# Optimization experiments

Measured on AMD Instinct MI355X. Metric: run time of the kernel, lower is better.

The kernel has to match this reference:

```python
import jax, jax.numpy as jnp
import numpy as np

B, T, L, H, NH, F, V, K = 8, 128, 12, 768, 12, 3072, 30522, 5
DH = H // NH
START, STOP = 3, 4  # tag_to_idx['<START>'], tag_to_idx['<STOP>']


def _ln(x, s, b):
    m = jnp.mean(x, -1, keepdims=True)
    v = jnp.var(x, -1, keepdims=True)
    return (x - m) * jax.lax.rsqrt(v + 1e-12) * s + b


def setup_inputs() -> dict:
    key = jax.random.key(0)
    ks = jax.random.split(key, 16)
    sc = 0.02
    rn = lambda k, shp: jax.random.normal(k, shp, jnp.float32) * sc
    inp = {
        'sentence': jax.random.randint(ks[0], (B, T), 0, V),
        'sentence_mask': jnp.ones((B, T), jnp.int32),
        'word_emb': rn(ks[1], (V, H)),
        'pos_emb': rn(ks[2], (T, H)),
        'type_emb': rn(ks[3], (2, H)),
        'emb_ln_s': jnp.ones((H,), jnp.float32),
        'emb_ln_b': jnp.zeros((H,), jnp.float32),
        'Wqkv': rn(ks[4], (L, H, 3 * H)), 'bqkv': jnp.zeros((L, 3 * H), jnp.float32),
        'Wo': rn(ks[5], (L, H, H)), 'bo': jnp.zeros((L, H), jnp.float32),
        'ln1_s': jnp.ones((L, H), jnp.float32), 'ln1_b': jnp.zeros((L, H), jnp.float32),
        'W1': rn(ks[6], (L, H, F)), 'b1': jnp.zeros((L, F), jnp.float32),
        'W2': rn(ks[7], (L, F, H)), 'b2': jnp.zeros((L, H), jnp.float32),
        'ln2_s': jnp.ones((L, H), jnp.float32), 'ln2_b': jnp.zeros((L, H), jnp.float32),
        'Wt': rn(ks[8], (H, K)), 'bt': jnp.zeros((K,), jnp.float32),
    }
    trans = jax.random.normal(ks[9], (K, K), jnp.float32)
    # transitions[START, :] = -10000 ; transitions[:, STOP] = -10000
    trans = trans.at[START, :].set(-10000.0).at[:, STOP].set(-10000.0)
    inp['transitions'] = trans
    return inp


def _bert_feats(sentence, sentence_mask, word_emb, pos_emb, type_emb,
                emb_ln_s, emb_ln_b, Wqkv, bqkv, Wo, bo, ln1_s, ln1_b,
                W1, b1, W2, b2, ln2_s, ln2_b, Wt, bt):
    # embeddings (token_type_ids=None -> all zeros)
    x = word_emb[sentence] + pos_emb[None, :, :] + type_emb[0][None, None, :]
    x = _ln(x, emb_ln_s, emb_ln_b)
    # additive attention bias from padding mask
    bias = (1.0 - sentence_mask.astype(jnp.float32))[:, None, None, :] * -10000.0
    inv_sqrt_dh = 1.0 / np.sqrt(DH)

    def layer(h, p):
        wqkv, bqk, wo, bo_, s1, sb1, w1, wb1, w2, wb2, s2, sb2 = p
        qkv = h @ wqkv + bqk
        q, k, v = jnp.split(qkv, 3, axis=-1)
        q = q.reshape(B, T, NH, DH)
        k = k.reshape(B, T, NH, DH)
        v = v.reshape(B, T, NH, DH)
        att = jnp.einsum('bqhd,bkhd->bhqk', q, k) * inv_sqrt_dh + bias
        att = jax.nn.softmax(att, axis=-1)
        ctx = jnp.einsum('bhqk,bkhd->bqhd', att, v).reshape(B, T, H)
        h = _ln(h + ctx @ wo + bo_, s1, sb1)
        ff = jax.nn.gelu(h @ w1 + wb1) @ w2 + wb2
        h = _ln(h + ff, s2, sb2)
        return h, None

    x, _ = jax.lax.scan(layer, x, (Wqkv, bqkv, Wo, bo, ln1_s, ln1_b,
                                   W1, b1, W2, b2, ln2_s, ln2_b))
    # dropout(p=0.2) is identity at inference
    return x @ Wt + bt  # [B, T, K]


def _viterbi(feats, transitions):
    # feats: [B, T, K]; transitions[to, from]
    init = jnp.full((B, K), -10000.0, feats.dtype).at[:, START].set(0.0)

    def fwd_step(ld, feat_t):
        m = transitions[None, :, :] + ld[:, None, :]  # [B, K(to), K(from)]
        best = jnp.max(m, axis=-1)
        psi_t = jnp.argmax(m, axis=-1)
        return best + feat_t, psi_t

    feats_t = jnp.swapaxes(feats, 0, 1)  # [T, B, K]
    ld, psis = jax.lax.scan(fwd_step, init, feats_t[1:])  # psis: [T-1, B, K]
    score = jnp.max(ld, axis=-1)          # [B]
    last = jnp.argmax(ld, axis=-1)        # [B]

    def bwd_step(p, psi_t):
        prev = jnp.take_along_axis(psi_t, p[:, None], axis=-1)[:, 0]
        return prev, prev

    _, rest = jax.lax.scan(bwd_step, last, psis, reverse=True)  # [T-1, B]
    path = jnp.concatenate([rest, last[None, :]], axis=0).T     # [B, T]
    return score, path


def reference(sentence, sentence_mask, word_emb, pos_emb, type_emb,
              emb_ln_s, emb_ln_b, Wqkv, bqkv, Wo, bo, ln1_s, ln1_b,
              W1, b1, W2, b2, ln2_s, ln2_b, Wt, bt, transitions):
    feats = _bert_feats(sentence, sentence_mask, word_emb, pos_emb, type_emb,
                        emb_ln_s, emb_ln_b, Wqkv, bqkv, Wo, bo, ln1_s, ln1_b,
                        W1, b1, W2, b2, ln2_s, ln2_b, Wt, bt)
    score, path = _viterbi(feats, transitions)
    return score, path
```

## Files before the change

kernel.cpp:

```cpp
#include <hip/hip_runtime.h>
#include <cstdint>
#include <cstddef>

#define BB 8
#define TT 128
#define LL 12
#define HH 768
#define NHH 12
#define DHH 64
#define FFI 3072
#define KT 5
#define START_TAG 3
#define MTOK (BB*TT)

typedef _Float16 f16x8 __attribute__((ext_vector_type(8)));
typedef _Float16 f16x4 __attribute__((ext_vector_type(4)));
typedef float f32x4 __attribute__((ext_vector_type(4)));

__device__ __forceinline__ void gl_lds16(const _Float16* g, _Float16* l) {
    __builtin_amdgcn_global_load_lds(
        (const __attribute__((address_space(1))) unsigned int*)g,
        (__attribute__((address_space(3))) unsigned int*)l, 16, 0, 0);
}

__device__ __forceinline__ float gelu_f(float x) {
    float c = 0.7978845608028654f * (x + 0.044715f * x * x * x);
    return 0.5f * x * (1.f + tanhf(c));
}

__device__ __forceinline__ void write_h_planes(const float* rowbuf, int tok,
                                               _Float16* dh, _Float16* dl, int c) {
    int kb = c >> 2;
    int rowm = tok & 127, mb = tok >> 7;
    int koct = c & 3;
    int p = rowm * 4 + (koct ^ (rowm & 3));
    size_t tb = ((size_t)(mb * 24 + kb)) * 4096;
    f16x8 vh, vl;
#pragma unroll
    for (int j = 0; j < 8; ++j) {
        float x = rowbuf[c * 8 + j];
        _Float16 hi = (_Float16)x;
        vh[j] = hi;
        vl[j] = (_Float16)((x - (float)hi) * 4096.f);
    }
    *(f16x8*)(dh + tb + (size_t)p * 8) = vh;
    *(f16x8*)(dl + tb + (size_t)p * 8) = vl;
}

__global__ __launch_bounds__(256) void embed_ln_kernel(
    const int* __restrict__ sentence,
    const float* __restrict__ word_emb,
    const float* __restrict__ pos_emb,
    const float* __restrict__ type_emb,
    const float* __restrict__ ln_s,
    const float* __restrict__ ln_b,
    float* __restrict__ h,
    _Float16* __restrict__ dh, _Float16* __restrict__ dl)
{
    int tok = blockIdx.x;
    int t = tok % TT;
    int id = sentence[tok];
    const float* we = word_emb + (size_t)id * HH;
    const float* pe = pos_emb + (size_t)t * HH;

    __shared__ float rowbuf[HH];
    __shared__ float rs_[4], rss_[4];
    float x[3];
    float s = 0.f, ss = 0.f;
#pragma unroll
    for (int i = 0; i < 3; ++i) {
        int d = threadIdx.x + i * 256;
        float v = we[d] + pe[d] + type_emb[d];
        x[i] = v; s += v; ss += v * v;
    }
    for (int o = 32; o; o >>= 1) { s += __shfl_down(s, o); ss += __shfl_down(ss, o); }
    int wid = threadIdx.x >> 6;
    if ((threadIdx.x & 63) == 0) { rs_[wid] = s; rss_[wid] = ss; }
    __syncthreads();
    s = rs_[0] + rs_[1] + rs_[2] + rs_[3];
    ss = rss_[0] + rss_[1] + rss_[2] + rss_[3];
    float mean = s * (1.f / HH);
    float var = ss * (1.f / HH) - mean * mean;
    float rstd = rsqrtf(var + 1e-12f);
#pragma unroll
    for (int i = 0; i < 3; ++i) {
        int d = threadIdx.x + i * 256;
        float y = (x[i] - mean) * rstd * ln_s[d] + ln_b[d];
        h[(size_t)tok * HH + d] = y;
        rowbuf[d] = y;
    }
    __syncthreads();
    if (threadIdx.x < 96) write_h_planes(rowbuf, tok, dh, dl, threadIdx.x);
}

__global__ __launch_bounds__(256) void add_ln_red_kernel(
    float* __restrict__ h, const float* __restrict__ parts,
    const float* __restrict__ bias,
    const float* __restrict__ ln_s, const float* __restrict__ ln_b,
    _Float16* __restrict__ dh, _Float16* __restrict__ dl)
{
    int tok = blockIdx.x;
    __shared__ float rowbuf[HH];
    __shared__ float rs_[4], rss_[4];
    float x[3];
    float s = 0.f, ss = 0.f;
#pragma unroll
    for (int i = 0; i < 3; ++i) {
        int d = threadIdx.x + i * 256;
        size_t idx = (size_t)tok * HH + d;
        float delta = parts[idx] + parts[idx + (size_t)MTOK * HH]
                    + parts[idx + 2 * (size_t)MTOK * HH] + parts[idx + 3 * (size_t)MTOK * HH]
                    + bias[d];
        float v = h[idx] + delta;
        x[i] = v; s += v; ss += v * v;
    }
    for (int o = 32; o; o >>= 1) { s += __shfl_down(s, o); ss += __shfl_down(ss, o); }
    int wid = threadIdx.x >> 6;
    if ((threadIdx.x & 63) == 0) { rs_[wid] = s; rss_[wid] = ss; }
    __syncthreads();
    s = rs_[0] + rs_[1] + rs_[2] + rs_[3];
    ss = rss_[0] + rss_[1] + rss_[2] + rss_[3];
    float mean = s * (1.f / HH);
    float var = ss * (1.f / HH) - mean * mean;
    float rstd = rsqrtf(var + 1e-12f);
#pragma unroll
    for (int i = 0; i < 3; ++i) {
        int d = threadIdx.x + i * 256;
        float y = (x[i] - mean) * rstd * ln_s[d] + ln_b[d];
        h[(size_t)tok * HH + d] = y;
        rowbuf[d] = y;
    }
    __syncthreads();
    if (threadIdx.x < 96) write_h_planes(rowbuf, tok, dh, dl, threadIdx.x);
}

__global__ __launch_bounds__(256) void wconv_kernel(
    const float* __restrict__ Wqkv, const float* __restrict__ Wo,
    const float* __restrict__ W1, const float* __restrict__ W2,
    _Float16* __restrict__ qh, _Float16* __restrict__ ql,
    _Float16* __restrict__ oh, _Float16* __restrict__ ol,
    _Float16* __restrict__ f1h, _Float16* __restrict__ f1l,
    _Float16* __restrict__ f2h, _Float16* __restrict__ f2l)
{
    int b = blockIdx.x;
    const float* src; _Float16 *dh, *dl; int N, kTi, idx;
    if (b < 864)       { idx = b;        src = Wqkv; dh = qh;  dl = ql;  N = 2304; kTi = 24; }
    else if (b < 1152) { idx = b - 864;  src = Wo;   dh = oh;  dl = ol;  N = 768;  kTi = 24; }
    else if (b < 2304) { idx = b - 1152; src = W1;   dh = f1h; dl = f1l; N = 3072; kTi = 24; }
    else               { idx = b - 2304; src = W2;   dh = f2h; dl = f2l; N = 768;  kTi = 96; }
    int nb = idx / kTi, kb = idx % kTi;

    __shared__ float tile[32][65];
    const float* s0 = src + (size_t)(kb * 32) * N + nb * 64;
#pragma unroll
    for (int i = 0; i < 8; ++i) {
        int q = threadIdx.x + i * 256;
        int kk = q >> 6, n = q & 63;
        tile[kk][n] = s0[(size_t)kk * N + n];
    }
    __syncthreads();
    int p = threadIdx.x;
    int n = p >> 2, koct = (p & 3) ^ (n & 3);
    f16x8 vh, vl;
#pragma unroll
    for (int j = 0; j < 8; ++j) {
        float x = tile[koct * 8 + j][n];
        _Float16 hi = (_Float16)x;
        vh[j] = hi;
        vl[j] = (_Float16)((x - (float)hi) * 4096.f);
    }
    size_t tb = (size_t)idx * 2048;
    *(f16x8*)(dh + tb + (size_t)p * 8) = vh;
    *(f16x8*)(dl + tb + (size_t)p * 8) = vl;
}

template<int MODE>
__global__ __launch_bounds__(256) void mfma_gemm(
    const _Float16* __restrict__ Ah, const _Float16* __restrict__ Al,
    const _Float16* __restrict__ Bh, const _Float16* __restrict__ Bl,
    const float* __restrict__ bias, float* __restrict__ outF,
    _Float16* __restrict__ o1h, _Float16* __restrict__ o1l,
    _Float16* __restrict__ o2h, _Float16* __restrict__ o2l,
    int N, int kTi, int kpz)
{
    constexpr bool TRANS = (MODE >= 2);
    __shared__ _Float16 lds[2][12288];
    int tid = threadIdx.x, lane = tid & 63, w = tid >> 6;
    int wm = w >> 1, wn = w & 1;
    int mb = blockIdx.y, nb = blockIdx.x;
    int ktBeg = TRANS ? 0 : blockIdx.z * kpz;
    int ktEnd = TRANS ? kTi : ktBeg + kpz;

    const _Float16 *aTh, *aTl, *bTh, *bTl;
    if constexpr (!TRANS) {
        aTh = Ah + (size_t)mb * kTi * 4096;
        aTl = Al + (size_t)mb * kTi * 4096;
        bTh = Bh + (size_t)nb * kTi * 2048;
        bTl = Bl + (size_t)nb * kTi * 2048;
    } else {
        aTh = Ah + (size_t)(2 * mb) * kTi * 2048;
        aTl = Al + (size_t)(2 * mb) * kTi * 2048;
        bTh = Bh + (size_t)(nb >> 1) * kTi * 4096 + (nb & 1) * 2048;
        bTl = Bl + (size_t)(nb >> 1) * kTi * 4096 + (nb & 1) * 2048;
    }

    f32x4 acch[4][2], accc[4][2];
#pragma unroll
    for (int i = 0; i < 4; ++i)
#pragma unroll
        for (int j = 0; j < 2; ++j) { acch[i][j] = (f32x4)0.f; accc[i][j] = (f32x4)0.f; }

    auto stage = [&](int buf, int kt) {
#pragma unroll
        for (int j = 0; j < 6; ++j) {
            int i = w * 6 + j;
            const _Float16* src;
            if constexpr (!TRANS) {
                if (i < 8)       src = aTh + (size_t)kt * 4096 + i * 512;
                else if (i < 16) src = aTl + (size_t)kt * 4096 + (i - 8) * 512;
                else if (i < 20) src = bTh + (size_t)kt * 2048 + (i - 16) * 512;
                else             src = bTl + (size_t)kt * 2048 + (i - 20) * 512;
            } else {
                if (i < 8)       src = aTh + (size_t)(i >> 2) * kTi * 2048 + (size_t)kt * 2048 + (i & 3) * 512;
                else if (i < 16) src = aTl + (size_t)((i - 8) >> 2) * kTi * 2048 + (size_t)kt * 2048 + ((i - 8) & 3) * 512;
                else if (i < 20) src = bTh + (size_t)kt * 4096 + (i - 16) * 512;
                else             src = bTl + (size_t)kt * 4096 + (i - 20) * 512;
            }
            gl_lds16(src + lane * 8, &lds[buf][i * 512]);
        }
    };

    stage(0, ktBeg);
    __syncthreads();
    int buf = 0;
    int lm = lane & 15, lk = lane >> 4;
    for (int kt = ktBeg; kt < ktEnd; ++kt) {
        if (kt + 1 < ktEnd) stage(buf ^ 1, kt + 1);
        const char* lb = (const char*)&lds[buf][0];
        f16x8 ahf[4], alf[4], bhf[2], blf[2];
#pragma unroll
        for (int mi = 0; mi < 4; ++mi) {
            int row = wm * 64 + mi * 16 + lm;
            int off = (row * 64 + lk * 16) ^ ((row & 3) << 4);
            ahf[mi] = *(const f16x8*)(lb + off);
            alf[mi] = *(const f16x8*)(lb + 8192 + off);
        }
#pragma unroll
        for (int ni = 0; ni < 2; ++ni) {
            int nr = wn * 32 + ni * 16 + lm;
            int off = (nr * 64 + lk * 16) ^ ((nr & 3) << 4);
            bhf[ni] = *(const f16x8*)(lb + 16384 + off);
            blf[ni] = *(const f16x8*)(lb + 20480 + off);
        }
#pragma unroll
        for (int mi = 0; mi < 4; ++mi)
#pragma unroll
            for (int ni = 0; ni < 2; ++ni) {
                acch[mi][ni] = __builtin_amdgcn_mfma_f32_16x16x32_f16(ahf[mi], bhf[ni], acch[mi][ni], 0, 0, 0);
                accc[mi][ni] = __builtin_amdgcn_mfma_f32_16x16x32_f16(ahf[mi], blf[ni], accc[mi][ni], 0, 0, 0);
                accc[mi][ni] = __builtin_amdgcn_mfma_f32_16x16x32_f16(alf[mi], bhf[ni], accc[mi][ni], 0, 0, 0);
            }
        __syncthreads();
        buf ^= 1;
    }

    const float inv = 1.0f / 4096.0f;
    if constexpr (MODE == 0) {
        float* Cz = outF + (size_t)blockIdx.z * 1024 * N;
#pragma unroll
        for (int mi = 0; mi < 4; ++mi)
#pragma unroll
            for (int ni = 0; ni < 2; ++ni) {
                int col = nb * 64 + wn * 32 + ni * 16 + lm;
                int r0 = mb * 128 + wm * 64 + mi * 16 + lk * 4;
#pragma unroll
                for (int j = 0; j < 4; ++j)
                    Cz[(size_t)(r0 + j) * N + col] = acch[mi][ni][j] + accc[mi][ni][j] * inv;
            }
    } else if constexpr (MODE == 2) {
        int region = mb / 6;
#pragma unroll
        for (int mi = 0; mi < 4; ++mi)
#pragma unroll
            for (int ni = 0; ni < 2; ++ni) {
                int n = mb * 128 + wm * 64 + mi * 16 + lk * 4;
                int tok = nb * 64 + wn * 32 + ni * 16 + lm;
                float4 bv = *(const float4*)(bias + n);
                float v[4];
#pragma unroll
                for (int j = 0; j < 4; ++j)
                    v[j] = acch[mi][ni][j] + accc[mi][ni][j] * inv + (&bv.x)[j];
                int b = tok >> 7, q = tok & 127;
                if (region < 2) {
                    int hh2 = (n >> 6) % 12, d = n & 63;
                    size_t img = (size_t)(b * 12 + hh2);
                    _Float16* dsth = (region == 0) ? o1h : o2h;
                    _Float16* dstl = (region == 0) ? o1l : o2l;
                    int byteo = q * 128 + ((d * 2) ^ ((q & 7) << 4));
                    f16x4 hi, lo;
#pragma unroll
                    for (int j = 0; j < 4; ++j) {
                        _Float16 hv = (_Float16)v[j];
                        hi[j] = hv; lo[j] = (_Float16)((v[j] - (float)hv) * 4096.f);
                    }
                    *(f16x4*)((char*)dsth + img * 16384 + byteo) = hi;
                    *(f16x4*)((char*)dstl + img * 16384 + byteo) = lo;
                } else {
                    int hh2 = (n - 1536) >> 6, d = n & 63;
                    float* vdst = outF + (size_t)(b * 12 + hh2) * 8192;
#pragma unroll
                    for (int j = 0; j < 4; ++j)
                        vdst[(size_t)(d + j) * 128 + q] = v[j];
                }
            }
    } else {
#pragma unroll
        for (int mi = 0; mi < 4; ++mi)
#pragma unroll
            for (int ni = 0; ni < 2; ++ni) {
                int n = mb * 128 + wm * 64 + mi * 16 + lk * 4;
                int tok = nb * 64 + wn * 32 + ni * 16 + lm;
                float4 bv = *(const float4*)(bias + n);
                int mbt = tok >> 7, rowm = tok & 127;
                int kb = n >> 5, koct = (n >> 3) & 3, half = (n >> 2) & 1;
                size_t eo = ((size_t)(mbt * 96 + kb)) * 4096
                          + (size_t)(rowm * 4 + (koct ^ (rowm & 3))) * 8 + half * 4;
                f16x4 hi, lo;
#pragma unroll
                for (int j = 0; j < 4; ++j) {
                    float x = gelu_f(acch[mi][ni][j] + accc[mi][ni][j] * inv + (&bv.x)[j]);
                    _Float16 hv = (_Float16)x;
                    hi[j] = hv; lo[j] = (_Float16)((x - (float)hv) * 4096.f);
                }
                *(f16x4*)(o1h + eo) = hi;
                *(f16x4*)(o1l + eo) = lo;
            }
    }
}

__global__ __launch_bounds__(256, 1) void attn_mfma(
    const _Float16* __restrict__ Qp_h, const _Float16* __restrict__ Qp_l,
    const _Float16* __restrict__ Kp_h, const _Float16* __restrict__ Kp_l,
    const float* __restrict__ vT, const int* __restrict__ mask,
    _Float16* __restrict__ cA_h, _Float16* __restrict__ cA_l)
{
    __shared__ __align__(16) char sm[98816];
    char* Kh = sm;            char* Klo = sm + 16384;
    char* Qh = sm + 32768;    char* Qlo = sm + 49152;
    char* Ph = sm;            char* Plo = sm + 32768;
    char* Vth = sm + 65536;   char* Vtl = sm + 81920;
    float* biasf = (float*)(sm + 98304);

    int bx = blockIdx.x; int b = bx / 12, h = bx % 12;
    int tid = threadIdx.x, lane = tid & 63, wv = tid >> 6;
    int lm = lane & 15, g = lane >> 4;
    const float inv = 1.0f / 4096.0f;

    {
        const _Float16* srcs[4] = { Kp_h + (size_t)bx * 8192, Kp_l + (size_t)bx * 8192,
                                    Qp_h + (size_t)bx * 8192, Qp_l + (size_t)bx * 8192 };
        char* dsts[4] = { Kh, Klo, Qh, Qlo };
#pragma unroll
        for (int p = 0; p < 4; ++p)
#pragma unroll
            for (int r = 0; r < 4; ++r) {
                int cbase = r * 256 + wv * 64;
                gl_lds16(srcs[p] + (size_t)(cbase + lane) * 8, (_Float16*)(dsts[p] + (size_t)cbase * 16));
            }
    }
    if (tid < 128) biasf[tid] = (1.f - (float)mask[b * 128 + tid]) * -10000.f;
    __syncthreads();

    f32x4 ah[8][2], ac[8][2];
#pragma unroll
    for (int i = 0; i < 8; ++i)
#pragma unroll
        for (int j = 0; j < 2; ++j) { ah[i][j] = (f32x4)0.f; ac[i][j] = (f32x4)0.f; }
#pragma unroll
    for (int ks = 0; ks < 2; ++ks) {
        f16x8 qf[2][2];
#pragma unroll
        for (int nf = 0; nf < 2; ++nf) {
            int q = wv * 32 + nf * 16 + lm;
            int off = (q * 128 + ks * 64 + g * 16) ^ ((q & 7) << 4);
            qf[nf][0] = *(const f16x8*)(Qh + off);
            qf[nf][1] = *(const f16x8*)(Qlo + off);
        }
#pragma unroll
        for (int mf = 0; mf < 8; ++mf) {
            int kt = mf * 16 + lm;
            int off = (kt * 128 + ks * 64 + g * 16) ^ ((kt & 7) << 4);
            f16x8 kh = *(const f16x8*)(Kh + off);
            f16x8 kl = *(const f16x8*)(Klo + off);
#pragma unroll
            for (int nf = 0; nf < 2; ++nf) {
                ah[mf][nf] = __builtin_amdgcn_mfma_f32_16x16x32_f16(kh, qf[nf][0], ah[mf][nf], 0, 0, 0);
                ac[mf][nf] = __builtin_amdgcn_mfma_f32_16x16x32_f16(kh, qf[nf][1], ac[mf][nf], 0, 0, 0);
                ac[mf][nf] = __builtin_amdgcn_mfma_f32_16x16x32_f16(kl, qf[nf][0], ac[mf][nf], 0, 0, 0);
            }
        }
    }

    float kb_[8][4];
#pragma unroll
    for (int mf = 0; mf < 8; ++mf)
#pragma unroll
        for (int jj = 0; jj < 4; ++jj) kb_[mf][jj] = biasf[mf * 16 + g * 4 + jj];

    float pv_[2][8][4], rs_[2];
#pragma unroll
    for (int nf = 0; nf < 2; ++nf) {
        float mx = -1e30f;
#pragma unroll
        for (int mf = 0; mf < 8; ++mf)
#pragma unroll
            for (int jj = 0; jj < 4; ++jj) {
                float s = (ah[mf][nf][jj] + ac[mf][nf][jj] * inv) * 0.125f + kb_[mf][jj];
                pv_[nf][mf][jj] = s;
                mx = fmaxf(mx, s);
            }
        mx = fmaxf(mx, __shfl_xor(mx, 16));
        mx = fmaxf(mx, __shfl_xor(mx, 32));
        float sum = 0.f;
#pragma unroll
        for (int mf = 0; mf < 8; ++mf)
#pragma unroll
            for (int jj = 0; jj < 4; ++jj) {
                float e = expf(pv_[nf][mf][jj] - mx);
                pv_[nf][mf][jj] = e;
                sum += e;
            }
        sum += __shfl_xor(sum, 16);
        sum += __shfl_xor(sum, 32);
        rs_[nf] = 1.f / sum;
    }
    __syncthreads();

#pragma unroll
    for (int nf = 0; nf < 2; ++nf) {
        int q = wv * 32 + nf * 16 + lm;
#pragma unroll
        for (int mf = 0; mf < 8; ++mf) {
            f16x4 hi, lo;
#pragma unroll
            for (int jj = 0; jj < 4; ++jj) {
                float p = pv_[nf][mf][jj] * rs_[nf];
                _Float16 hv = (_Float16)p;
                hi[jj] = hv; lo[jj] = (_Float16)((p - (float)hv) * 4096.f);
            }
            int byteo = (q * 256 + mf * 32 + g * 8) ^ ((q & 7) << 4);
            *(f16x4*)(Ph + byteo) = hi;
            *(f16x4*)(Plo + byteo) = lo;
        }
    }
    {
        int d = tid >> 2, tb = (tid & 3) * 32;
        const float* vsrc = vT + (size_t)bx * 8192 + (size_t)d * 128 + tb;
#pragma unroll
        for (int i = 0; i < 8; ++i) {
            float4 v = *(const float4*)(vsrc + i * 4);
            f16x4 hi, lo;
#pragma unroll
            for (int jj = 0; jj < 4; ++jj) {
                float x = (&v.x)[jj];
                _Float16 hv = (_Float16)x;
                hi[jj] = hv; lo[jj] = (_Float16)((x - (float)hv) * 4096.f);
            }
            int byteo = (d * 256 + (tb + i * 4) * 2) ^ ((d & 7) << 4);
            *(f16x4*)(Vth + byteo) = hi;
            *(f16x4*)(Vtl + byteo) = lo;
        }
    }
    __syncthreads();

    f32x4 ch[4][2], cc[4][2];
#pragma unroll
    for (int i = 0; i < 4; ++i)
#pragma unroll
        for (int j = 0; j < 2; ++j) { ch[i][j] = (f32x4)0.f; cc[i][j] = (f32x4)0.f; }
#pragma unroll
    for (int ks = 0; ks < 4; ++ks) {
        f16x8 pf[2][2];
#pragma unroll
        for (int nf = 0; nf < 2; ++nf) {
            int q = wv * 32 + nf * 16 + lm;
            int off = (q * 256 + ks * 64 + g * 16) ^ ((q & 7) << 4);
            pf[nf][0] = *(const f16x8*)(Ph + off);
            pf[nf][1] = *(const f16x8*)(Plo + off);
        }
#pragma unroll
        for (int mf = 0; mf < 4; ++mf) {
            int d = mf * 16 + lm;
            int off = (d * 256 + ks * 64 + g * 16) ^ ((d & 7) << 4);
            f16x8 vh = *(const f16x8*)(Vth + off);
            f16x8 vl = *(const f16x8*)(Vtl + off);
#pragma unroll
            for (int nf = 0; nf < 2; ++nf) {
                ch[mf][nf] = __builtin_amdgcn_mfma_f32_16x16x32_f16(vh, pf[nf][0], ch[mf][nf], 0, 0, 0);
                cc[mf][nf] = __builtin_amdgcn_mfma_f32_16x16x32_f16(vh, pf[nf][1], cc[mf][nf], 0, 0, 0);
                cc[mf][nf] = __builtin_amdgcn_mfma_f32_16x16x32_f16(vl, pf[nf][0], cc[mf][nf], 0, 0, 0);
            }
        }
    }

#pragma unroll
    for (int mf = 0; mf < 4; ++mf)
#pragma unroll
        for (int nf = 0; nf < 2; ++nf) {
            int q = wv * 32 + nf * 16 + lm;
            int d0 = mf * 16 + g * 4;
            f16x4 hi, lo;
#pragma unroll
            for (int jj = 0; jj < 4; ++jj) {
                float x = ch[mf][nf][jj] + cc[mf][nf][jj] * inv;
                _Float16 hv = (_Float16)x;
                hi[jj] = hv; lo[jj] = (_Float16)((x - (float)hv) * 4096.f);
            }
            int kb = h * 2 + (d0 >> 5), koct = (d0 >> 3) & 3, half = (d0 >> 2) & 1;
            size_t eo = ((size_t)(b * 24 + kb)) * 4096
                      + (size_t)(q * 4 + (koct ^ (q & 3))) * 8 + half * 4;
            *(f16x4*)(cA_h + eo) = hi;
            *(f16x4*)(cA_l + eo) = lo;
        }
}

__global__ __launch_bounds__(320) void feats_kernel(
    const float* __restrict__ h, const float* __restrict__ Wt,
    const float* __restrict__ bt, float* __restrict__ feats)
{
    int tok = blockIdx.x;
    int w = threadIdx.x / 64, lane = threadIdx.x % 64;
    float s = 0.f;
    for (int d = lane; d < HH; d += 64)
        s += h[(size_t)tok * HH + d] * Wt[d * KT + w];
    for (int o = 32; o; o >>= 1) s += __shfl_down(s, o);
    if (lane == 0) feats[tok * KT + w] = s + bt[w];
}

__global__ __launch_bounds__(64) void viterbi_kernel(
    const float* __restrict__ feats, const float* __restrict__ trans,
    float* __restrict__ out)
{
    __shared__ float tr[KT][KT];
    __shared__ unsigned char psi[TT - 1][BB][KT];
    int tid = threadIdx.x;
    if (tid < KT * KT) tr[tid / KT][tid % KT] = trans[tid];
    __syncthreads();
    if (tid < BB) {
        int b = tid;
        float ld[KT];
#pragma unroll
        for (int k = 0; k < KT; ++k) ld[k] = (k == START_TAG) ? 0.f : -10000.f;
        for (int t = 1; t < TT; ++t) {
            float nld[KT];
#pragma unroll
            for (int to = 0; to < KT; ++to) {
                float best = tr[to][0] + ld[0];
                int arg = 0;
#pragma unroll
                for (int fr = 1; fr < KT; ++fr) {
                    float v = tr[to][fr] + ld[fr];
                    if (v > best) { best = v; arg = fr; }
                }
                psi[t - 1][b][to] = (unsigned char)arg;
                nld[to] = best + feats[(size_t)(b * TT + t) * KT + to];
            }
#pragma unroll
            for (int k = 0; k < KT; ++k) ld[k] = nld[k];
        }
        float sc = ld[0]; int last = 0;
#pragma unroll
        for (int k = 1; k < KT; ++k) if (ld[k] > sc) { sc = ld[k]; last = k; }
        out[b] = sc;
        int p = last;
        out[BB + b * TT + (TT - 1)] = (float)last;
        for (int t = TT - 2; t >= 0; --t) {
            p = psi[t][b][p];
            out[BB + b * TT + t] = (float)p;
        }
    }
}

extern "C" void kernel_launch(void* const* d_in, const int* in_sizes, int n_in,
                              void* d_out, int out_size, void* d_ws, size_t ws_size,
                              hipStream_t stream) {
    const int*   sentence = (const int*)d_in[0];
    const int*   mask     = (const int*)d_in[1];
    const float* word_emb = (const float*)d_in[2];
    const float* pos_emb  = (const float*)d_in[3];
    const float* type_emb = (const float*)d_in[4];
    const float* emb_ln_s = (const float*)d_in[5];
    const float* emb_ln_b = (const float*)d_in[6];
    const float* Wqkv     = (const float*)d_in[7];
    const float* bqkv     = (const float*)d_in[8];
    const float* Wo       = (const float*)d_in[9];
    const float* bo       = (const float*)d_in[10];
    const float* ln1_s    = (const float*)d_in[11];
    const float* ln1_b    = (const float*)d_in[12];
    const float* W1       = (const float*)d_in[13];
    const float* b1       = (const float*)d_in[14];
    const float* W2       = (const float*)d_in[15];
    const float* b2       = (const float*)d_in[16];
    const float* ln2_s    = (const float*)d_in[17];
    const float* ln2_b    = (const float*)d_in[18];
    const float* Wt       = (const float*)d_in[19];
    const float* bt       = (const float*)d_in[20];
    const float* trans    = (const float*)d_in[21];

    char* base = (char*)d_ws;
    size_t off = 0;
    auto alloc = [&](size_t bytes) { void* p = base + off; off += (bytes + 255) & ~(size_t)255; return p; };

    _Float16* wq_h = (_Float16*)alloc(768u * 2304 * 2);
    _Float16* wq_l = (_Float16*)alloc(768u * 2304 * 2);
    _Float16* wo_h = (_Float16*)alloc(768u * 768 * 2);
    _Float16* wo_l = (_Float16*)alloc(768u * 768 * 2);
    _Float16* w1_h = (_Float16*)alloc(768u * 3072 * 2);
    _Float16* w1_l = (_Float16*)alloc(768u * 3072 * 2);
    _Float16* w2_h = (_Float16*)alloc(3072u * 768 * 2);
    _Float16* w2_l = (_Float16*)alloc(3072u * 768 * 2);
    float* h       = (float*)alloc((size_t)MTOK * HH * 4);
    _Float16* hA_h = (_Float16*)alloc((size_t)MTOK * HH * 2);
    _Float16* hA_l = (_Float16*)alloc((size_t)MTOK * HH * 2);
    _Float16* Qp_h = (_Float16*)alloc((size_t)96 * 8192 * 2);
    _Float16* Qp_l = (_Float16*)alloc((size_t)96 * 8192 * 2);
    _Float16* Kp_h = (_Float16*)alloc((size_t)96 * 8192 * 2);
    _Float16* Kp_l = (_Float16*)alloc((size_t)96 * 8192 * 2);
    float* vT      = (float*)alloc((size_t)96 * 8192 * 4);
    _Float16* cA_h = (_Float16*)alloc((size_t)MTOK * HH * 2);
    _Float16* cA_l = (_Float16*)alloc((size_t)MTOK * HH * 2);
    _Float16* gA_h = (_Float16*)alloc((size_t)MTOK * FFI * 2);
    _Float16* gA_l = (_Float16*)alloc((size_t)MTOK * FFI * 2);
    float* parts   = (float*)alloc((size_t)4 * MTOK * HH * 4);
    float* featsb  = (float*)alloc((size_t)MTOK * KT * 4);

    embed_ln_kernel<<<MTOK, 256, 0, stream>>>(sentence, word_emb, pos_emb, type_emb,
                                              emb_ln_s, emb_ln_b, h, hA_h, hA_l);
    for (int l = 0; l < LL; ++l) {
        wconv_kernel<<<3456, 256, 0, stream>>>(
            Wqkv + (size_t)l * 768 * 2304, Wo + (size_t)l * 768 * 768,
            W1 + (size_t)l * 768 * 3072, W2 + (size_t)l * 3072 * 768,
            wq_h, wq_l, wo_h, wo_l, w1_h, w1_l, w2_h, w2_l);
        mfma_gemm<2><<<dim3(16, 18), 256, 0, stream>>>(
            wq_h, wq_l, hA_h, hA_l, bqkv + (size_t)l * 2304, vT,
            Qp_h, Qp_l, Kp_h, Kp_l, 0, 24, 24);
        attn_mfma<<<96, 256, 0, stream>>>(Qp_h, Qp_l, Kp_h, Kp_l, vT, mask, cA_h, cA_l);
        mfma_gemm<0><<<dim3(12, 8, 4), 256, 0, stream>>>(
            cA_h, cA_l, wo_h, wo_l, nullptr, parts,
            nullptr, nullptr, nullptr, nullptr, 768, 24, 6);
        add_ln_red_kernel<<<MTOK, 256, 0, stream>>>(
            h, parts, bo + (size_t)l * HH, ln1_s + (size_t)l * HH, ln1_b + (size_t)l * HH, hA_h, hA_l);
        mfma_gemm<3><<<dim3(16, 24), 256, 0, stream>>>(
            w1_h, w1_l, hA_h, hA_l, b1 + (size_t)l * FFI, nullptr,
            gA_h, gA_l, nullptr, nullptr, 0, 24, 24);
        mfma_gemm<0><<<dim3(12, 8, 4), 256, 0, stream>>>(
            gA_h, gA_l, w2_h, w2_l, nullptr, parts,
            nullptr, nullptr, nullptr, nullptr, 768, 96, 24);
        add_ln_red_kernel<<<MTOK, 256, 0, stream>>>(
            h, parts, b2 + (size_t)l * HH, ln2_s + (size_t)l * HH, ln2_b + (size_t)l * HH, hA_h, hA_l);
    }
    feats_kernel<<<MTOK, 320, 0, stream>>>(h, Wt, bt, featsb);
    viterbi_kernel<<<1, 64, 0, stream>>>(featsb, trans, (float*)d_out);
}
```

Baseline: 1.496 ms.

## Batch weight conversion for all layers and fuse final LN with tag projection

When the workspace is large enough, all twelve layers' fp32 weights are split into fp16 hi/lo planes by a single up-front conversion launch instead of one launch per layer. This removes eleven launches and lets the conversion run as one large grid. The last layer's add+LayerNorm kernel is also templated to compute the 5-tag emission features directly, which drops the separate feats kernel and the final h write. The cost is a much larger workspace footprint, and the GEMM row-stride arguments change from 0 to explicit values, which may alter how the weight operand is addressed.

```diff
diff --git a/kernel.cpp b/kernel.cpp
--- a/kernel.cpp
+++ b/kernel.cpp
@@ -12,6 +12,11 @@
 #define KT 5
 #define START_TAG 3
 #define MTOK (BB*TT)
+
+#define LQS 1769472u
+#define LOS 589824u
+#define L1S 2359296u
+#define L2S 2359296u
 
 typedef _Float16 f16x8 __attribute__((ext_vector_type(8)));
 typedef _Float16 f16x4 __attribute__((ext_vector_type(4)));
@@ -93,11 +98,14 @@
     if (threadIdx.x < 96) write_h_planes(rowbuf, tok, dh, dl, threadIdx.x);
 }
 
+template<int FEATS>
 __global__ __launch_bounds__(256) void add_ln_red_kernel(
     float* __restrict__ h, const float* __restrict__ parts,
     const float* __restrict__ bias,
     const float* __restrict__ ln_s, const float* __restrict__ ln_b,
-    _Float16* __restrict__ dh, _Float16* __restrict__ dl)
+    _Float16* __restrict__ dh, _Float16* __restrict__ dl,
+    const float* __restrict__ Wt, const float* __restrict__ bt,
+    float* __restrict__ feats)
 {
     int tok = blockIdx.x;
     __shared__ float rowbuf[HH];
@@ -123,17 +131,45 @@
     float mean = s * (1.f / HH);
     float var = ss * (1.f / HH) - mean * mean;
     float rstd = rsqrtf(var + 1e-12f);
+    float yv[3];
 #pragma unroll
     for (int i = 0; i < 3; ++i) {
         int d = threadIdx.x + i * 256;
         float y = (x[i] - mean) * rstd * ln_s[d] + ln_b[d];
-        h[(size_t)tok * HH + d] = y;
-        rowbuf[d] = y;
-    }
-    __syncthreads();
-    if (threadIdx.x < 96) write_h_planes(rowbuf, tok, dh, dl, threadIdx.x);
-}
-
+        yv[i] = y;
+        if constexpr (!FEATS) {
+            h[(size_t)tok * HH + d] = y;
+            rowbuf[d] = y;
+        }
+    }
+    if constexpr (!FEATS) {
+        __syncthreads();
+        if (threadIdx.x < 96) write_h_planes(rowbuf, tok, dh, dl, threadIdx.x);
+    } else {
+        float pt[5] = {0.f, 0.f, 0.f, 0.f, 0.f};
+#pragma unroll
+        for (int i = 0; i < 3; ++i) {
+            int d = threadIdx.x + i * 256;
+#pragma unroll
+            for (int t = 0; t < 5; ++t) pt[t] += yv[i] * Wt[d * 5 + t];
+        }
+#pragma unroll
+        for (int t = 0; t < 5; ++t)
+            for (int o = 32; o; o >>= 1) pt[t] += __shfl_down(pt[t], o);
+        __shared__ float fred[4][5];
+        if ((threadIdx.x & 63) == 0)
+#pragma unroll
+            for (int t = 0; t < 5; ++t) fred[wid][t] = pt[t];
+        __syncthreads();
+        if (threadIdx.x < 5) {
+            float fs = fred[0][threadIdx.x] + fred[1][threadIdx.x]
+                     + fred[2][threadIdx.x] + fred[3][threadIdx.x] + bt[threadIdx.x];
+            feats[tok * 5 + threadIdx.x] = fs;
+        }
+    }
+}
+
+template<int ALL>
 __global__ __launch_bounds__(256) void wconv_kernel(
     const float* __restrict__ Wqkv, const float* __restrict__ Wo,
     const float* __restrict__ W1, const float* __restrict__ W2,
@@ -142,12 +178,14 @@
     _Float16* __restrict__ f1h, _Float16* __restrict__ f1l,
     _Float16* __restrict__ f2h, _Float16* __restrict__ f2l)
 {
-    int b = blockIdx.x;
+    int bb = blockIdx.x;
+    int l = ALL ? bb / 3456 : 0;
+    int b = ALL ? bb % 3456 : bb;
     const float* src; _Float16 *dh, *dl; int N, kTi, idx;
-    if (b < 864)       { idx = b;        src = Wqkv; dh = qh;  dl = ql;  N = 2304; kTi = 24; }
-    else if (b < 1152) { idx = b - 864;  src = Wo;   dh = oh;  dl = ol;  N = 768;  kTi = 24; }
-    else if (b < 2304) { idx = b - 1152; src = W1;   dh = f1h; dl = f1l; N = 3072; kTi = 24; }
-    else               { idx = b - 2304; src = W2;   dh = f2h; dl = f2l; N = 768;  kTi = 96; }
+    if (b < 864)       { idx = b;        src = Wqkv + (size_t)l * 768 * 2304; dh = qh  + (size_t)l * LQS; dl = ql  + (size_t)l * LQS; N = 2304; kTi = 24; }
+    else if (b < 1152) { idx = b - 864;  src = Wo   + (size_t)l * 768 * 768;  dh = oh  + (size_t)l * LOS; dl = ol  + (size_t)l * LOS; N = 768;  kTi = 24; }
+    else if (b < 2304) { idx = b - 1152; src = W1   + (size_t)l * 768 * 3072; dh = f1h + (size_t)l * L1S; dl = f1l + (size_t)l * L1S; N = 3072; kTi = 24; }
+    else               { idx = b - 2304; src = W2   + (size_t)l * 3072 * 768; dh = f2h + (size_t)l * L2S; dl = f2l + (size_t)l * L2S; N = 768;  kTi = 96; }
     int nb = idx / kTi, kb = idx % kTi;
 
     __shared__ float tile[32][65];
@@ -522,19 +560,6 @@
             *(f16x4*)(cA_h + eo) = hi;
             *(f16x4*)(cA_l + eo) = lo;
         }
-}
-
-__global__ __launch_bounds__(320) void feats_kernel(
-    const float* __restrict__ h, const float* __restrict__ Wt,
-    const float* __restrict__ bt, float* __restrict__ feats)
-{
-    int tok = blockIdx.x;
-    int w = threadIdx.x / 64, lane = threadIdx.x % 64;
-    float s = 0.f;
-    for (int d = lane; d < HH; d += 64)
-        s += h[(size_t)tok * HH + d] * Wt[d * KT + w];
-    for (int o = 32; o; o >>= 1) s += __shfl_down(s, o);
-    if (lane == 0) feats[tok * KT + w] = s + bt[w];
 }
 
 __global__ __launch_bounds__(64) void viterbi_kernel(
@@ -611,14 +636,17 @@
     size_t off = 0;
     auto alloc = [&](size_t bytes) { void* p = base + off; off += (bytes + 255) & ~(size_t)255; return p; };
 
-    _Float16* wq_h = (_Float16*)alloc(768u * 2304 * 2);
-    _Float16* wq_l = (_Float16*)alloc(768u * 2304 * 2);
-    _Float16* wo_h = (_Float16*)alloc(768u * 768 * 2);
-    _Float16* wo_l = (_Float16*)alloc(768u * 768 * 2);
-    _Float16* w1_h = (_Float16*)alloc(768u * 3072 * 2);
-    _Float16* w1_l = (_Float16*)alloc(768u * 3072 * 2);
-    _Float16* w2_h = (_Float16*)alloc(3072u * 768 * 2);
-    _Float16* w2_l = (_Float16*)alloc(3072u * 768 * 2);
+    bool allL = ws_size >= (384ULL << 20);
+    int NLL = allL ? 12 : 1;
+
+    _Float16* wq_h = (_Float16*)alloc((size_t)LQS * NLL * 2);
+    _Float16* wq_l = (_Float16*)alloc((size_t)LQS * NLL * 2);
+    _Float16* wo_h = (_Float16*)alloc((size_t)LOS * NLL * 2);
+    _Float16* wo_l = (_Float16*)alloc((size_t)LOS * NLL * 2);
+    _Float16* w1_h = (_Float16*)alloc((size_t)L1S * NLL * 2);
+    _Float16* w1_l = (_Float16*)alloc((size_t)L1S * NLL * 2);
+    _Float16* w2_h = (_Float16*)alloc((size_t)L2S * NLL * 2);
+    _Float16* w2_l = (_Float16*)alloc((size_t)L2S * NLL * 2);
     float* h       = (float*)alloc((size_t)MTOK * HH * 4);
     _Float16* hA_h = (_Float16*)alloc((size_t)MTOK * HH * 2);
     _Float16* hA_l = (_Float16*)alloc((size_t)MTOK * HH * 2);
@@ -636,29 +664,46 @@
 
     embed_ln_kernel<<<MTOK, 256, 0, stream>>>(sentence, word_emb, pos_emb, type_emb,
                                               emb_ln_s, emb_ln_b, h, hA_h, hA_l);
+    if (allL) {
+        wconv_kernel<1><<<41472, 256, 0, stream>>>(
+            Wqkv, Wo, W1, W2, wq_h, wq_l, wo_h, wo_l, w1_h, w1_l, w2_h, w2_l);
+    }
     for (int l = 0; l < LL; ++l) {
-        wconv_kernel<<<3456, 256, 0, stream>>>(
-            Wqkv + (size_t)l * 768 * 2304, Wo + (size_t)l * 768 * 768,
-            W1 + (size_t)l * 768 * 3072, W2 + (size_t)l * 3072 * 768,
-            wq_h, wq_l, wo_h, wo_l, w1_h, w1_l, w2_h, w2_l);
+        size_t qO  = allL ? (size_t)l * LQS : 0;
+        size_t oO  = allL ? (size_t)l * LOS : 0;
+        size_t f1O = allL ? (size_t)l * L1S : 0;
+        size_t f2O = allL ? (size_t)l * L2S : 0;
+        if (!allL) {
+            wconv_kernel<0><<<3456, 256, 0, stream>>>(
+                Wqkv + (size_t)l * 768 * 2304, Wo + (size_t)l * 768 * 768,
+                W1 + (size_t)l * 768 * 3072, W2 + (size_t)l * 3072 * 768,
+                wq_h, wq_l, wo_h, wo_l, w1_h, w1_l, w2_h, w2_l);
+        }
         mfma_gemm<2><<<dim3(16, 18), 256, 0, stream>>>(
-            wq_h, wq_l, hA_h, hA_l, bqkv + (size_t)l * 2304, vT,
-            Qp_h, Qp_l, Kp_h, Kp_l, 0, 24, 24);
+            wq_h + qO, wq_l + qO, hA_h, hA_l, bqkv + (size_t)l * 2304, vT,
+            Qp_h, Qp_l, Kp_h, Kp_l, 2304, 24, 24);
         attn_mfma<<<96, 256, 0, stream>>>(Qp_h, Qp_l, Kp_h, Kp_l, vT, mask, cA_h, cA_l);
         mfma_gemm<0><<<dim3(12, 8, 4), 256, 0, stream>>>(
-            cA_h, cA_l, wo_h, wo_l, nullptr, parts,
+            cA_h, cA_l, wo_h + oO, wo_l + oO, nullptr, parts,
             nullptr, nullptr, nullptr, nullptr, 768, 24, 6);
-        add_ln_red_kernel<<<MTOK, 256, 0, stream>>>(
-            h, parts, bo + (size_t)l * HH, ln1_s + (size_t)l * HH, ln1_b + (size_t)l * HH, hA_h, hA_l);
+        add_ln_red_kernel<0><<<MTOK, 256, 0, stream>>>(
+            h, parts, bo + (size_t)l * HH, ln1_s + (size_t)l * HH, ln1_b + (size_t)l * HH,
+            hA_h, hA_l, nullptr, nullptr, nullptr);
         mfma_gemm<3><<<dim3(16, 24), 256, 0, stream>>>(
-            w1_h, w1_l, hA_h, hA_l, b1 + (size_t)l * FFI, nullptr,
-            gA_h, gA_l, nullptr, nullptr, 0, 24, 24);
+            w1_h + f1O, w1_l + f1O, hA_h, hA_l, b1 + (size_t)l * FFI, nullptr,
+            gA_h, gA_l, nullptr, nullptr, 3072, 24, 24);
         mfma_gemm<0><<<dim3(12, 8, 4), 256, 0, stream>>>(
-            gA_h, gA_l, w2_h, w2_l, nullptr, parts,
+            gA_h, gA_l, w2_h + f2O, w2_l + f2O, nullptr, parts,
             nullptr, nullptr, nullptr, nullptr, 768, 96, 24);
-        add_ln_red_kernel<<<MTOK, 256, 0, stream>>>(
-            h, parts, b2 + (size_t)l * HH, ln2_s + (size_t)l * HH, ln2_b + (size_t)l * HH, hA_h, hA_l);
-    }
-    feats_kernel<<<MTOK, 320, 0, stream>>>(h, Wt, bt, featsb);
+        if (l < LL - 1) {
+            add_ln_red_kernel<0><<<MTOK, 256, 0, stream>>>(
+                h, parts, b2 + (size_t)l * HH, ln2_s + (size_t)l * HH, ln2_b + (size_t)l * HH,
+                hA_h, hA_l, nullptr, nullptr, nullptr);
+        } else {
+            add_ln_red_kernel<1><<<MTOK, 256, 0, stream>>>(
+                h, parts, b2 + (size_t)l * HH, ln2_s + (size_t)l * HH, ln2_b + (size_t)l * HH,
+                hA_h, hA_l, Wt, bt, featsb);
+        }
+    }
     viterbi_kernel<<<1, 64, 0, stream>>>(featsb, trans, (float*)d_out);
 }
```

After: 1.646 ms. 10.0% more time.
